# Performance work log

Hardware: AMD Instinct MI355X
Metric: run time of the kernel (lower is better)

## Reference

```python
import jax, jax.numpy as jnp
import numpy as np

B, S, D = 1, 2048, 2048
HQ, HKV, HD = 32, 8, 64
EXPAND = HQ // HKV

def _rotate_half(x):
    x1, x2 = x[..., : x.shape[-1] // 2], x[..., x.shape[-1] // 2 :]
    return jnp.concatenate((-x2, x1), axis=-1)

def setup_inputs() -> dict:
    key = jax.random.key(0)
    k1, k2, k3 = jax.random.split(key, 3)
    hidden_states = jax.random.normal(k1, (B, S, D), dtype=jnp.float32)
    # Llama weight init scale ~ small
    Wq = jax.random.normal(k2, (HQ * HD, D), dtype=jnp.float32) * 0.02
    Wk = jax.random.normal(k3, (HKV * HD, D), dtype=jnp.float32) * 0.02
    # true rotary cos/sin tables, shape [B, S, HD]
    inv_freq = 1.0 / (10000.0 ** (jnp.arange(0, HD, 2, dtype=jnp.float32) / HD))
    pos = jnp.arange(S, dtype=jnp.float32)
    freqs = pos[:, None] * inv_freq[None, :]            # [S, HD/2]
    emb = jnp.concatenate((freqs, freqs), axis=-1)       # [S, HD]
    cos = jnp.broadcast_to(jnp.cos(emb)[None], (B, S, HD))
    sin = jnp.broadcast_to(jnp.sin(emb)[None], (B, S, HD))
    attn_mask = jnp.zeros((B, 1, S, S), dtype=jnp.float32)  # accepted but unused by the module
    return {"hidden_states": hidden_states, "cos": cos, "sin": sin,
            "attn_mask": attn_mask, "Wq": Wq, "Wk": Wk}

def reference(hidden_states, cos, sin, attn_mask, Wq, Wk):
    b, s, _ = hidden_states.shape
    # projections (nn.Linear, no bias): x @ W.T
    q = hidden_states @ Wq.T                              # [b, s, HQ*HD]
    k = hidden_states @ Wk.T                              # [b, s, HKV*HD]
    q = q.reshape(b, s, HQ, HD).transpose(0, 2, 1, 3)     # [b, HQ, s, HD]
    k = k.reshape(b, s, HKV, HD).transpose(0, 2, 1, 3)    # [b, HKV, s, HD]
    c = cos[:, None, :, :]                                # unsqueeze_dim=1
    sn = sin[:, None, :, :]
    q = q * c + _rotate_half(q) * sn
    k = k * c + _rotate_half(k) * sn
    k = jnp.repeat(k, EXPAND, axis=1)                     # GQA repeat_interleave -> [b, HQ, s, HD]
    scores = jnp.einsum('bhqd,bhkd->bhqk', q, k)          # NO 1/sqrt(d) scaling (faithful)
    return jax.nn.softmax(scores, axis=-1)
```

## Files before the change

kernel.cpp:

```cpp
#include <hip/hip_runtime.h>
#include <hip/hip_bf16.h>

typedef _Float16 half8 __attribute__((ext_vector_type(8)));
typedef float floatx4 __attribute__((ext_vector_type(4)));

#define SEQ 2048
#define DIM 2048
#define HQ 32
#define HKV 8
#define HD 64
#define NQ (HQ*HD)
#define NK (HKV*HD)
#define NTOT (NQ+NK)

__global__ void convert_kernel(const float* __restrict__ X,
                               const float* __restrict__ Wq,
                               const float* __restrict__ Wk,
                               _Float16* __restrict__ Xh,
                               _Float16* __restrict__ Wh) {
    long i = (long)blockIdx.x * 256 + threadIdx.x;
    const long nx = (long)SEQ * DIM;
    const long nw = (long)NTOT * DIM;
    if (i < nx) {
        Xh[i] = (_Float16)X[i];
    } else if (i < nx + nw) {
        long j = i - nx;
        float v = (j < (long)NQ * DIM) ? Wq[j] : Wk[j - (long)NQ * DIM];
        Wh[j] = (_Float16)v;
    }
}

__global__ __launch_bounds__(256) void gemm1_kernel(
    const _Float16* __restrict__ Xh, const _Float16* __restrict__ Wh,
    const float* __restrict__ cosb, const float* __restrict__ sinb,
    _Float16* __restrict__ qout, _Float16* __restrict__ kout)
{
    __shared__ __align__(16) _Float16 lsA[128 * 32];
    __shared__ __align__(16) _Float16 lsB[128 * 32];
    const int tid  = threadIdx.x;
    const int lane = tid & 63;
    const int wv   = tid >> 6;
    const int wm   = wv & 1, wn = wv >> 1;
    const int m    = lane & 15, quad = lane >> 4;
    const int s0   = blockIdx.x * 128;
    const int n0   = blockIdx.y * 128;

    floatx4 acc[4][4];
    #pragma unroll
    for (int i = 0; i < 4; i++)
        #pragma unroll
        for (int j = 0; j < 4; j++)
            acc[i][j] = floatx4{0.f, 0.f, 0.f, 0.f};

    for (int k0 = 0; k0 < DIM; k0 += 32) {
        __syncthreads();
        #pragma unroll
        for (int t = 0; t < 2; t++) {
            int c  = tid + t * 256;
            int r  = c >> 2;
            int cc = c & 3;
            *(uint4*)(lsA + r * 32 + cc * 8) =
                *(const uint4*)(Xh + (long)(s0 + r) * DIM + k0 + cc * 8);
            *(uint4*)(lsB + r * 32 + cc * 8) =
                *(const uint4*)(Wh + (long)(n0 + r) * DIM + k0 + cc * 8);
        }
        __syncthreads();

        half8 aF[4], bF[4];
        #pragma unroll
        for (int i = 0; i < 4; i++)
            aF[i] = *(const half8*)(lsA + (wm * 64 + i * 16 + m) * 32 + quad * 8);
        #pragma unroll
        for (int j = 0; j < 4; j++)
            bF[j] = *(const half8*)(lsB + (wn * 64 + j * 16 + m) * 32 + quad * 8);
        #pragma unroll
        for (int i = 0; i < 4; i++)
            #pragma unroll
            for (int j = 0; j < 4; j++)
                acc[i][j] = __builtin_amdgcn_mfma_f32_16x16x32_f16(
                    aF[i], bF[j], acc[i][j], 0, 0, 0);
    }

    #pragma unroll
    for (int i = 0; i < 4; i++) {
        #pragma unroll
        for (int reg = 0; reg < 4; reg++) {
            int s = s0 + wm * 64 + i * 16 + quad * 4 + reg;
            #pragma unroll
            for (int j = 0; j < 4; j++) {
                int col = n0 + wn * 64 + j * 16 + m;
                int d   = j * 16 + m;
                float v = acc[i][j][reg];
                float partner = (j < 2) ? -acc[i][j + 2][reg] : acc[i][j - 2][reg];
                float cs = cosb[s * HD + d];
                float sn = sinb[s * HD + d];
                _Float16 o = (_Float16)(v * cs + partner * sn);
                if (col < NQ) {
                    int hq = col >> 6;
                    qout[((long)hq * SEQ + s) * HD + d] = o;
                } else {
                    int hk = (col - NQ) >> 6;
                    kout[((long)hk * SEQ + s) * HD + d] = o;
                }
            }
        }
    }
}

__global__ __launch_bounds__(512) void attn_kernel(
    const _Float16* __restrict__ qf, const _Float16* __restrict__ kf,
    float* __restrict__ out)
{
    __shared__ float redm[8][16];
    __shared__ float redl[8][16];
    const int tid  = threadIdx.x;
    const int lane = tid & 63;
    const int w    = tid >> 6;
    const int m    = lane & 15, quad = lane >> 4;
    const int qb   = blockIdx.x;
    const int h    = blockIdx.y;
    const int kvh  = h >> 2;
    const int s0   = qb * 16;

    const _Float16* qbase = qf + ((long)h * SEQ + s0) * HD;
    const _Float16* kbase = kf + (long)kvh * SEQ * HD;

    half8 aF0 = *(const half8*)(qbase + (long)m * HD + quad * 8);
    half8 aF1 = *(const half8*)(qbase + (long)m * HD + 32 + quad * 8);

    floatx4 acc[16];
    #pragma unroll
    for (int ct = 0; ct < 16; ct++) {
        int n0 = w * 256 + ct * 16;
        const _Float16* kp = kbase + (long)(n0 + m) * HD + quad * 8;
        half8 bF0 = *(const half8*)(kp);
        half8 bF1 = *(const half8*)(kp + 32);
        floatx4 a = floatx4{0.f, 0.f, 0.f, 0.f};
        a = __builtin_amdgcn_mfma_f32_16x16x32_f16(aF0, bF0, a, 0, 0, 0);
        a = __builtin_amdgcn_mfma_f32_16x16x32_f16(aF1, bF1, a, 0, 0, 0);
        acc[ct] = a;
    }

    float gm[4], inv[4];
    #pragma unroll
    for (int r = 0; r < 4; r++) {
        float lm = acc[0][r];
        #pragma unroll
        for (int ct = 1; ct < 16; ct++) lm = fmaxf(lm, acc[ct][r]);
        for (int off = 1; off < 16; off <<= 1)
            lm = fmaxf(lm, __shfl_xor(lm, off));
        if (m == 0) redm[w][quad * 4 + r] = lm;
    }
    __syncthreads();
    #pragma unroll
    for (int r = 0; r < 4; r++) {
        int row = quad * 4 + r;
        float g = redm[0][row];
        #pragma unroll
        for (int ww = 1; ww < 8; ww++) g = fmaxf(g, redm[ww][row]);
        gm[r] = g;
    }
    #pragma unroll
    for (int r = 0; r < 4; r++) {
        float ls = 0.f;
        #pragma unroll
        for (int ct = 0; ct < 16; ct++) {
            float e = __expf(acc[ct][r] - gm[r]);
            acc[ct][r] = e;
            ls += e;
        }
        for (int off = 1; off < 16; off <<= 1)
            ls += __shfl_xor(ls, off);
        if (m == 0) redl[w][quad * 4 + r] = ls;
    }
    __syncthreads();
    #pragma unroll
    for (int r = 0; r < 4; r++) {
        int row = quad * 4 + r;
        float t = 0.f;
        #pragma unroll
        for (int ww = 0; ww < 8; ww++) t += redl[ww][row];
        inv[r] = 1.0f / t;
    }
    float* obase = out + ((long)h * SEQ + s0) * SEQ;
    #pragma unroll
    for (int ct = 0; ct < 16; ct++) {
        int n0 = w * 256 + ct * 16;
        #pragma unroll
        for (int r = 0; r < 4; r++) {
            int row = quad * 4 + r;
            obase[(long)row * SEQ + n0 + m] = acc[ct][r] * inv[r];
        }
    }
}

extern "C" void kernel_launch(void* const* d_in, const int* in_sizes, int n_in,
                              void* d_out, int out_size, void* d_ws, size_t ws_size,
                              hipStream_t stream) {
    const float* hidden = (const float*)d_in[0];
    const float* cosb   = (const float*)d_in[1];
    const float* sinb   = (const float*)d_in[2];
    const float* Wq     = (const float*)d_in[4];
    const float* Wk     = (const float*)d_in[5];
    float* out = (float*)d_out;

    char* ws = (char*)d_ws;
    _Float16* Xh = (_Float16*)ws;
    _Float16* Wh = (_Float16*)(ws + 8388608);
    _Float16* qf = (_Float16*)(ws + 8388608 + 10485760);
    _Float16* kf = (_Float16*)(ws + 8388608 + 10485760 + 8388608);

    convert_kernel<<<36864, 256, 0, stream>>>(hidden, Wq, Wk, Xh, Wh);
    gemm1_kernel<<<dim3(16, 20), 256, 0, stream>>>(Xh, Wh, cosb, sinb, qf, kf);
    attn_kernel<<<dim3(128, 32), 512, 0, stream>>>(qf, kf, out);
}
```

Baseline: 703.2 us.

## Vectorize conversion, use direct-to-LDS swizzled loads in GEMM, transpose attention MFMA for vector stores

The fp32-to-fp16 conversion now handles 8 elements per thread with float4 loads and one 16-byte store. The projection GEMM moves to 64x128 tiles with a 64-wide K step, loading tiles with global_load_lds and an XOR swizzle to avoid LDS bank conflicts, and launches twice as many blocks. The attention kernel swaps the MFMA operands so each lane holds four consecutive key columns of one query row. This lets the softmax reductions use only two cross-lane shuffles and the output be written as 16-byte vector stores instead of scalar ones.

```diff
diff --git a/kernel.cpp b/kernel.cpp
--- a/kernel.cpp
+++ b/kernel.cpp
@@ -13,21 +13,33 @@
 #define NK (HKV*HD)
 #define NTOT (NQ+NK)
 
-__global__ void convert_kernel(const float* __restrict__ X,
-                               const float* __restrict__ Wq,
-                               const float* __restrict__ Wk,
-                               _Float16* __restrict__ Xh,
-                               _Float16* __restrict__ Wh) {
-    long i = (long)blockIdx.x * 256 + threadIdx.x;
-    const long nx = (long)SEQ * DIM;
-    const long nw = (long)NTOT * DIM;
-    if (i < nx) {
-        Xh[i] = (_Float16)X[i];
-    } else if (i < nx + nw) {
-        long j = i - nx;
-        float v = (j < (long)NQ * DIM) ? Wq[j] : Wk[j - (long)NQ * DIM];
-        Wh[j] = (_Float16)v;
-    }
+#define GLOAD_LDS16(g, l) \
+    __builtin_amdgcn_global_load_lds( \
+        (const __attribute__((address_space(1))) void*)(g), \
+        (__attribute__((address_space(3))) void*)(l), 16, 0, 0)
+
+__global__ __launch_bounds__(256) void convert_kernel(
+    const float* __restrict__ X, const float* __restrict__ Wq,
+    const float* __restrict__ Wk, _Float16* __restrict__ Xh,
+    _Float16* __restrict__ Wh)
+{
+    const long c   = (long)blockIdx.x * 256 + threadIdx.x;
+    const long nxc = (long)SEQ * DIM / 8;
+    const float* src;
+    _Float16* dst;
+    if (c < nxc) {
+        src = X + c * 8;
+        dst = Xh + c * 8;
+    } else {
+        long f = (c - nxc) * 8;
+        src = (f < (long)NQ * DIM) ? Wq + f : Wk + (f - (long)NQ * DIM);
+        dst = Wh + f;
+    }
+    float4 a = ((const float4*)src)[0];
+    float4 b = ((const float4*)src)[1];
+    half8 h = {(_Float16)a.x, (_Float16)a.y, (_Float16)a.z, (_Float16)a.w,
+               (_Float16)b.x, (_Float16)b.y, (_Float16)b.z, (_Float16)b.w};
+    *(half8*)dst = h;
 }
 
 __global__ __launch_bounds__(256) void gemm1_kernel(
@@ -35,57 +47,72 @@
     const float* __restrict__ cosb, const float* __restrict__ sinb,
     _Float16* __restrict__ qout, _Float16* __restrict__ kout)
 {
-    __shared__ __align__(16) _Float16 lsA[128 * 32];
-    __shared__ __align__(16) _Float16 lsB[128 * 32];
+    __shared__ __align__(16) _Float16 lsA[64 * 64];
+    __shared__ __align__(16) _Float16 lsB[128 * 64];
     const int tid  = threadIdx.x;
     const int lane = tid & 63;
     const int wv   = tid >> 6;
     const int wm   = wv & 1, wn = wv >> 1;
     const int m    = lane & 15, quad = lane >> 4;
-    const int s0   = blockIdx.x * 128;
+    const int s0   = blockIdx.x * 64;
     const int n0   = blockIdx.y * 128;
 
-    floatx4 acc[4][4];
-    #pragma unroll
-    for (int i = 0; i < 4; i++)
+    floatx4 acc[2][4];
+    #pragma unroll
+    for (int i = 0; i < 2; i++)
         #pragma unroll
         for (int j = 0; j < 4; j++)
             acc[i][j] = floatx4{0.f, 0.f, 0.f, 0.f};
 
-    for (int k0 = 0; k0 < DIM; k0 += 32) {
+    for (int k0 = 0; k0 < DIM; k0 += 64) {
         __syncthreads();
         #pragma unroll
-        for (int t = 0; t < 2; t++) {
-            int c  = tid + t * 256;
-            int r  = c >> 2;
-            int cc = c & 3;
-            *(uint4*)(lsA + r * 32 + cc * 8) =
-                *(const uint4*)(Xh + (long)(s0 + r) * DIM + k0 + cc * 8);
-            *(uint4*)(lsB + r * 32 + cc * 8) =
-                *(const uint4*)(Wh + (long)(n0 + r) * DIM + k0 + cc * 8);
+        for (int r = 0; r < 2; r++) {
+            int c    = r * 256 + tid;
+            int row  = c >> 3;
+            int chg  = (c & 7) ^ (row & 7);
+            GLOAD_LDS16(Xh + (long)(s0 + row) * DIM + k0 + chg * 8,
+                        (char*)lsA + (r * 256 + wv * 64) * 16);
+        }
+        #pragma unroll
+        for (int r = 0; r < 4; r++) {
+            int c    = r * 256 + tid;
+            int row  = c >> 3;
+            int chg  = (c & 7) ^ (row & 7);
+            GLOAD_LDS16(Wh + (long)(n0 + row) * DIM + k0 + chg * 8,
+                        (char*)lsB + (r * 256 + wv * 64) * 16);
         }
         __syncthreads();
 
-        half8 aF[4], bF[4];
-        #pragma unroll
-        for (int i = 0; i < 4; i++)
-            aF[i] = *(const half8*)(lsA + (wm * 64 + i * 16 + m) * 32 + quad * 8);
-        #pragma unroll
-        for (int j = 0; j < 4; j++)
-            bF[j] = *(const half8*)(lsB + (wn * 64 + j * 16 + m) * 32 + quad * 8);
-        #pragma unroll
-        for (int i = 0; i < 4; i++)
-            #pragma unroll
-            for (int j = 0; j < 4; j++)
-                acc[i][j] = __builtin_amdgcn_mfma_f32_16x16x32_f16(
-                    aF[i], bF[j], acc[i][j], 0, 0, 0);
-    }
-
-    #pragma unroll
-    for (int i = 0; i < 4; i++) {
+        #pragma unroll
+        for (int kk = 0; kk < 2; kk++) {
+            half8 aF[2], bF[4];
+            #pragma unroll
+            for (int i = 0; i < 2; i++) {
+                int row = wm * 32 + i * 16 + m;
+                int pc  = ((kk << 2) | quad) ^ (m & 7);
+                aF[i] = *(const half8*)(lsA + row * 64 + pc * 8);
+            }
+            #pragma unroll
+            for (int j = 0; j < 4; j++) {
+                int row = wn * 64 + j * 16 + m;
+                int pc  = ((kk << 2) | quad) ^ (m & 7);
+                bF[j] = *(const half8*)(lsB + row * 64 + pc * 8);
+            }
+            #pragma unroll
+            for (int i = 0; i < 2; i++)
+                #pragma unroll
+                for (int j = 0; j < 4; j++)
+                    acc[i][j] = __builtin_amdgcn_mfma_f32_16x16x32_f16(
+                        aF[i], bF[j], acc[i][j], 0, 0, 0);
+        }
+    }
+
+    #pragma unroll
+    for (int i = 0; i < 2; i++) {
         #pragma unroll
         for (int reg = 0; reg < 4; reg++) {
-            int s = s0 + wm * 64 + i * 16 + quad * 4 + reg;
+            int s = s0 + wm * 32 + i * 16 + quad * 4 + reg;
             #pragma unroll
             for (int j = 0; j < 4; j++) {
                 int col = n0 + wn * 64 + j * 16 + m;
@@ -125,72 +152,60 @@
     const _Float16* qbase = qf + ((long)h * SEQ + s0) * HD;
     const _Float16* kbase = kf + (long)kvh * SEQ * HD;
 
-    half8 aF0 = *(const half8*)(qbase + (long)m * HD + quad * 8);
-    half8 aF1 = *(const half8*)(qbase + (long)m * HD + 32 + quad * 8);
+    half8 bQ0 = *(const half8*)(qbase + (long)m * HD + quad * 8);
+    half8 bQ1 = *(const half8*)(qbase + (long)m * HD + 32 + quad * 8);
 
     floatx4 acc[16];
     #pragma unroll
     for (int ct = 0; ct < 16; ct++) {
         int n0 = w * 256 + ct * 16;
         const _Float16* kp = kbase + (long)(n0 + m) * HD + quad * 8;
-        half8 bF0 = *(const half8*)(kp);
-        half8 bF1 = *(const half8*)(kp + 32);
+        half8 aK0 = *(const half8*)(kp);
+        half8 aK1 = *(const half8*)(kp + 32);
         floatx4 a = floatx4{0.f, 0.f, 0.f, 0.f};
-        a = __builtin_amdgcn_mfma_f32_16x16x32_f16(aF0, bF0, a, 0, 0, 0);
-        a = __builtin_amdgcn_mfma_f32_16x16x32_f16(aF1, bF1, a, 0, 0, 0);
+        a = __builtin_amdgcn_mfma_f32_16x16x32_f16(aK0, bQ0, a, 0, 0, 0);
+        a = __builtin_amdgcn_mfma_f32_16x16x32_f16(aK1, bQ1, a, 0, 0, 0);
         acc[ct] = a;
     }
 
-    float gm[4], inv[4];
-    #pragma unroll
-    for (int r = 0; r < 4; r++) {
-        float lm = acc[0][r];
-        #pragma unroll
-        for (int ct = 1; ct < 16; ct++) lm = fmaxf(lm, acc[ct][r]);
-        for (int off = 1; off < 16; off <<= 1)
-            lm = fmaxf(lm, __shfl_xor(lm, off));
-        if (m == 0) redm[w][quad * 4 + r] = lm;
-    }
+    float lm = acc[0][0];
+    #pragma unroll
+    for (int ct = 0; ct < 16; ct++)
+        #pragma unroll
+        for (int r = 0; r < 4; r++) lm = fmaxf(lm, acc[ct][r]);
+    lm = fmaxf(lm, __shfl_xor(lm, 16));
+    lm = fmaxf(lm, __shfl_xor(lm, 32));
+    if (quad == 0) redm[w][m] = lm;
     __syncthreads();
-    #pragma unroll
-    for (int r = 0; r < 4; r++) {
-        int row = quad * 4 + r;
-        float g = redm[0][row];
-        #pragma unroll
-        for (int ww = 1; ww < 8; ww++) g = fmaxf(g, redm[ww][row]);
-        gm[r] = g;
-    }
-    #pragma unroll
-    for (int r = 0; r < 4; r++) {
-        float ls = 0.f;
-        #pragma unroll
-        for (int ct = 0; ct < 16; ct++) {
-            float e = __expf(acc[ct][r] - gm[r]);
+    float g = redm[0][m];
+    #pragma unroll
+    for (int ww = 1; ww < 8; ww++) g = fmaxf(g, redm[ww][m]);
+
+    float ls = 0.f;
+    #pragma unroll
+    for (int ct = 0; ct < 16; ct++) {
+        #pragma unroll
+        for (int r = 0; r < 4; r++) {
+            float e = __expf(acc[ct][r] - g);
             acc[ct][r] = e;
             ls += e;
         }
-        for (int off = 1; off < 16; off <<= 1)
-            ls += __shfl_xor(ls, off);
-        if (m == 0) redl[w][quad * 4 + r] = ls;
-    }
+    }
+    ls += __shfl_xor(ls, 16);
+    ls += __shfl_xor(ls, 32);
+    if (quad == 0) redl[w][m] = ls;
     __syncthreads();
-    #pragma unroll
-    for (int r = 0; r < 4; r++) {
-        int row = quad * 4 + r;
-        float t = 0.f;
-        #pragma unroll
-        for (int ww = 0; ww < 8; ww++) t += redl[ww][row];
-        inv[r] = 1.0f / t;
-    }
-    float* obase = out + ((long)h * SEQ + s0) * SEQ;
+    float tot = 0.f;
+    #pragma unroll
+    for (int ww = 0; ww < 8; ww++) tot += redl[ww][m];
+    float inv = 1.0f / tot;
+
+    float* obase = out + ((long)h * SEQ + s0 + m) * SEQ + w * 256 + quad * 4;
     #pragma unroll
     for (int ct = 0; ct < 16; ct++) {
-        int n0 = w * 256 + ct * 16;
-        #pragma unroll
-        for (int r = 0; r < 4; r++) {
-            int row = quad * 4 + r;
-            obase[(long)row * SEQ + n0 + m] = acc[ct][r] * inv[r];
-        }
+        floatx4 v = acc[ct];
+        v[0] *= inv; v[1] *= inv; v[2] *= inv; v[3] *= inv;
+        *(floatx4*)(obase + ct * 16) = v;
     }
 }
 
@@ -210,7 +225,7 @@
     _Float16* qf = (_Float16*)(ws + 8388608 + 10485760);
     _Float16* kf = (_Float16*)(ws + 8388608 + 10485760 + 8388608);
 
-    convert_kernel<<<36864, 256, 0, stream>>>(hidden, Wq, Wk, Xh, Wh);
-    gemm1_kernel<<<dim3(16, 20), 256, 0, stream>>>(Xh, Wh, cosb, sinb, qf, kf);
+    convert_kernel<<<4608, 256, 0, stream>>>(hidden, Wq, Wk, Xh, Wh);
+    gemm1_kernel<<<dim3(32, 20), 256, 0, stream>>>(Xh, Wh, cosb, sinb, qf, kf);
     attn_kernel<<<dim3(128, 32), 512, 0, stream>>>(qf, kf, out);
 }
```

After: 686.0 us. 2.5% less time.
